# Optimization experiments

Hardware: AMD Instinct MI355X
Metric: run time of the kernel (lower is better)

## Reference

```python
import jax, jax.numpy as jnp
import numpy as np

B, T, I, H, C = 8192, 784, 1, 30, 10


def setup_inputs() -> dict:
    key = jax.random.key(0)
    ks = jax.random.split(key, 7)
    s_ih = 1.0 / np.sqrt(H)
    return {
        "x": jax.random.normal(ks[0], (B, T, I), dtype=jnp.float32),
        "W_ih": jax.random.uniform(ks[1], (H, I), jnp.float32, -s_ih, s_ih),
        "W_hh": jax.random.uniform(ks[2], (H, H), jnp.float32, -s_ih, s_ih),
        "b_ih": jax.random.uniform(ks[3], (H,), jnp.float32, -s_ih, s_ih),
        "b_hh": jax.random.uniform(ks[4], (H,), jnp.float32, -s_ih, s_ih),
        "W_fc": jax.random.uniform(ks[5], (C, H), jnp.float32, -s_ih, s_ih),
        "b_fc": jax.random.uniform(ks[6], (C,), jnp.float32, -s_ih, s_ih),
    }


def reference(x, W_ih, W_hh, b_ih, b_hh, W_fc, b_fc):
    # x: [B, T, I] -> scan over time. h_t = tanh(x_t W_ih^T + b_ih + h W_hh^T + b_hh)
    xs = jnp.swapaxes(x, 0, 1)  # [T, B, I]
    h0 = jnp.zeros((x.shape[0], W_hh.shape[0]), dtype=x.dtype)
    bias = b_ih + b_hh  # [H]

    def step(h, xt):
        h_new = jnp.tanh(xt @ W_ih.T + h @ W_hh.T + bias)
        return h_new, None

    hT, _ = jax.lax.scan(step, h0, xs)  # hT: [B, H] == out[:, -1, :]
    return hT @ W_fc.T + b_fc  # [B, C]
```

## Files before the change

kernel.cpp:

```cpp
#include <hip/hip_runtime.h>


#define BB 8192
#define TT 784
#define HH 30
#define CC 10

typedef __attribute__((ext_vector_type(8))) short  bf16x8;
typedef __attribute__((ext_vector_type(4))) float  f32x4;
typedef __attribute__((ext_vector_type(4))) unsigned uint4v;

__device__ __forceinline__ float tanh_pre(float s) {
    return 1.0f - 2.0f * __builtin_amdgcn_rcpf(__expf(s) + 1.0f);
}

#define BPAIR(p0, p1, hp, lp) do {                                          \
    asm("v_cvt_pk_bf16_f32 %0, %1, %2" : "=v"(hp) : "v"(p0), "v"(p1));      \
    const float _h0 = __uint_as_float((hp) << 16);                          \
    const float _h1 = __uint_as_float((hp) & 0xffff0000u);                  \
    const float _l0 = (p0) - _h0;                                           \
    const float _l1 = (p1) - _h1;                                           \
    asm("v_cvt_pk_bf16_f32 %0, %1, %2" : "=v"(lp) : "v"(_l0), "v"(_l1));    \
} while (0)

__global__ __launch_bounds__(64)
__attribute__((amdgpu_waves_per_eu(1, 1)))
void rnn_scan_kernel(const float* __restrict__ x,
                     const float* __restrict__ W_ih,
                     const float* __restrict__ W_hh,
                     const float* __restrict__ b_ih,
                     const float* __restrict__ b_hh,
                     const float* __restrict__ W_fc,
                     const float* __restrict__ b_fc,
                     float* __restrict__ out) {
    const int lane = threadIdx.x & 63;
    const int n    = lane & 15;
    const int g    = lane >> 4;
    const int b    = blockIdx.x * 16 + n;

    const int r1 = 8 * (n >> 2) + (n & 3);
    const int r2 = r1 + 4;
    unsigned a1h[4], a1l[4], a2h[4], a2l[4];
#pragma unroll
    for (int d = 0; d < 4; ++d) {
        const int k0 = 8 * g + 2 * d, k1 = k0 + 1;
        const float w1a = (k0 < HH) ? 2.0f * W_hh[r1 * HH + k0] : 0.f;
        const float w1b = (k1 < HH) ? 2.0f * W_hh[r1 * HH + k1] : 0.f;
        const float w2a = (r2 < HH && k0 < HH) ? 2.0f * W_hh[r2 * HH + k0] : 0.f;
        const float w2b = (r2 < HH && k1 < HH) ? 2.0f * W_hh[r2 * HH + k1] : 0.f;
        const unsigned u1a = __float_as_uint(w1a), u1b = __float_as_uint(w1b);
        const unsigned u2a = __float_as_uint(w2a), u2b = __float_as_uint(w2b);
        a1h[d] = (u1b & 0xffff0000u) | (u1a >> 16);
        a2h[d] = (u2b & 0xffff0000u) | (u2a >> 16);
        const float l1a = w1a - __uint_as_float(u1a & 0xffff0000u);
        const float l1b = w1b - __uint_as_float(u1b & 0xffff0000u);
        const float l2a = w2a - __uint_as_float(u2a & 0xffff0000u);
        const float l2b = w2b - __uint_as_float(u2b & 0xffff0000u);
        a1l[d] = (__float_as_uint(l1b) & 0xffff0000u) | (__float_as_uint(l1a) >> 16);
        a2l[d] = (__float_as_uint(l2b) & 0xffff0000u) | (__float_as_uint(l2a) >> 16);
    }
    bf16x8 A1h = __builtin_bit_cast(bf16x8, (uint4v){a1h[0], a1h[1], a1h[2], a1h[3]});
    bf16x8 A1l = __builtin_bit_cast(bf16x8, (uint4v){a1l[0], a1l[1], a1l[2], a1l[3]});
    bf16x8 A2h = __builtin_bit_cast(bf16x8, (uint4v){a2h[0], a2h[1], a2h[2], a2h[3]});
    bf16x8 A2l = __builtin_bit_cast(bf16x8, (uint4v){a2l[0], a2l[1], a2l[2], a2l[3]});
    asm volatile("" : "+v"(A1h), "+v"(A1l), "+v"(A2h), "+v"(A2l));

    float bias1[4], wih1[4], bias2[4], wih2[4];
#pragma unroll
    for (int r = 0; r < 4; ++r) {
        const int q1 = 8 * g + r;
        bias1[r] = 2.0f * (b_ih[q1] + b_hh[q1]);
        wih1[r]  = 2.0f * W_ih[q1];
        const int q2 = q1 + 4;
        bias2[r] = (q2 < HH) ? 2.0f * (b_ih[q2] + b_hh[q2]) : 0.f;
        wih2[r]  = (q2 < HH) ? 2.0f * W_ih[q2] : 0.f;
        asm volatile("" : "+v"(bias1[r]), "+v"(wih1[r]), "+v"(bias2[r]), "+v"(wih2[r]));
    }

    float h0 = 0.f, h1 = 0.f, h2 = 0.f, h3 = 0.f;
    float h4 = 0.f, h5 = 0.f, h6 = 0.f, h7 = 0.f;

    const float* xp = x + (size_t)b * TT;
    const int NQ = TT / 4;
    float4 xq = *(const float4*)xp;
    float4 xn = *(const float4*)(xp + 4);

    for (int qq = 0; qq < NQ; ++qq) {
        const float4 xf = (qq + 2 < NQ) ? *(const float4*)(xp + (qq + 2) * 4)
                                        : make_float4(0.f, 0.f, 0.f, 0.f);
#pragma unroll
        for (int u = 0; u < 4; ++u) {
            const float xt = (u == 0) ? xq.x : (u == 1) ? xq.y
                           : (u == 2) ? xq.z : xq.w;
            f32x4 accP1 = { fmaf(xt, wih1[0], bias1[0]), fmaf(xt, wih1[1], bias1[1]),
                            fmaf(xt, wih1[2], bias1[2]), fmaf(xt, wih1[3], bias1[3]) };
            f32x4 accP2 = { fmaf(xt, wih2[0], bias2[0]), fmaf(xt, wih2[1], bias2[1]),
                            fmaf(xt, wih2[2], bias2[2]), fmaf(xt, wih2[3], bias2[3]) };
            unsigned bh0, bh1, bh2, bh3, bl0, bl1, bl2, bl3;
            BPAIR(h0, h1, bh0, bl0);
            BPAIR(h2, h3, bh1, bl1);
            BPAIR(h4, h5, bh2, bl2);
            BPAIR(h6, h7, bh3, bl3);
            const bf16x8 Bh = __builtin_bit_cast(bf16x8, (uint4v){bh0, bh1, bh2, bh3});
            const bf16x8 Bl = __builtin_bit_cast(bf16x8, (uint4v){bl0, bl1, bl2, bl3});
            const f32x4 zed = {0.f, 0.f, 0.f, 0.f};
            accP1 = __builtin_amdgcn_mfma_f32_16x16x32_bf16(A1h, Bh, accP1, 0, 0, 0);
            accP2 = __builtin_amdgcn_mfma_f32_16x16x32_bf16(A2h, Bh, accP2, 0, 0, 0);
            f32x4 q1 = __builtin_amdgcn_mfma_f32_16x16x32_bf16(A1h, Bl, zed, 0, 0, 0);
            f32x4 q2 = __builtin_amdgcn_mfma_f32_16x16x32_bf16(A2h, Bl, zed, 0, 0, 0);
            q1 = __builtin_amdgcn_mfma_f32_16x16x32_bf16(A1l, Bh, q1, 0, 0, 0);
            q2 = __builtin_amdgcn_mfma_f32_16x16x32_bf16(A2l, Bh, q2, 0, 0, 0);
            const f32x4 s1 = accP1 + q1;
            const f32x4 s2 = accP2 + q2;
            h0 = tanh_pre(s1[0]); h1 = tanh_pre(s1[1]);
            h2 = tanh_pre(s1[2]); h3 = tanh_pre(s1[3]);
            h4 = tanh_pre(s2[0]); h5 = tanh_pre(s2[1]);
            h6 = tanh_pre(s2[2]); h7 = tanh_pre(s2[3]);
        }
        xq = xn;
        xn = xf;
    }

    const float hreg[8] = {h0, h1, h2, h3, h4, h5, h6, h7};
#pragma unroll
    for (int c = 0; c < CC; ++c) {
        float p = 0.f;
#pragma unroll
        for (int j = 0; j < 8; ++j) {
            const int k = 8 * g + j;
            if (k < HH) p = fmaf(W_fc[c * HH + k], hreg[j], p);
        }
        p += __shfl_xor(p, 16);
        p += __shfl_xor(p, 32);
        if (g == 0) out[(size_t)b * CC + c] = p + b_fc[c];
    }
}

extern "C" void kernel_launch(void* const* d_in, const int* in_sizes, int n_in,
                              void* d_out, int out_size, void* d_ws, size_t ws_size,
                              hipStream_t stream) {
    const float* x    = (const float*)d_in[0];
    const float* W_ih = (const float*)d_in[1];
    const float* W_hh = (const float*)d_in[2];
    const float* b_ih = (const float*)d_in[3];
    const float* b_hh = (const float*)d_in[4];
    const float* W_fc = (const float*)d_in[5];
    const float* b_fc = (const float*)d_in[6];

    hipLaunchKernelGGL(rnn_scan_kernel,
                       dim3(BB / 16), dim3(64), 0, stream,
                       x, W_ih, W_hh, b_ih, b_hh, W_fc, b_fc,
                       (float*)d_out);
}
```

Measured before the change: 287.2 us.

## Split hidden rows across two waves with LDS exchange of bf16 state

Each block now runs two waves, and each wave computes half of the hidden rows (one MFMA set instead of two). The packed bf16 hi/lo hidden state is exchanged through double-buffered shared memory with a block barrier every timestep. The weights are prescaled by 2/ln2 so tanh can use the exp2 builtin directly instead of __expf. The goal is to halve the per-wave serial MFMA and tanh latency per step, at the cost of an LDS round-trip and __syncthreads on the critical recurrence path.

```diff
diff --git a/kernel.cpp b/kernel.cpp
--- a/kernel.cpp
+++ b/kernel.cpp
@@ -10,8 +10,16 @@
 typedef __attribute__((ext_vector_type(4))) float  f32x4;
 typedef __attribute__((ext_vector_type(4))) unsigned uint4v;
 
-__device__ __forceinline__ float tanh_pre(float s) {
-    return 1.0f - 2.0f * __builtin_amdgcn_rcpf(__expf(s) + 1.0f);
+#if __has_builtin(__builtin_amdgcn_exp2f)
+#define EXP2(v) __builtin_amdgcn_exp2f(v)
+#else
+#define EXP2(v) __expf((v) * 0.69314718055994531f)
+#endif
+
+#define SCL 2.8853900817779268f
+
+__device__ __forceinline__ float tanh_e2(float s) {
+    return 1.0f - 2.0f * __builtin_amdgcn_rcpf(EXP2(s) + 1.0f);
 }
 
 #define BPAIR(p0, p1, hp, lp) do {                                          \
@@ -23,7 +31,7 @@
     asm("v_cvt_pk_bf16_f32 %0, %1, %2" : "=v"(lp) : "v"(_l0), "v"(_l1));    \
 } while (0)
 
-__global__ __launch_bounds__(64)
+__global__ __launch_bounds__(128)
 __attribute__((amdgpu_waves_per_eu(1, 1)))
 void rnn_scan_kernel(const float* __restrict__ x,
                      const float* __restrict__ W_ih,
@@ -33,52 +41,44 @@
                      const float* __restrict__ W_fc,
                      const float* __restrict__ b_fc,
                      float* __restrict__ out) {
-    const int lane = threadIdx.x & 63;
+    __shared__ unsigned long long Ehi[2][64][2];
+    __shared__ unsigned long long Elo[2][64][2];
+    __shared__ float hfc[16][33];
+
+    const int tid  = threadIdx.x;
+    const int wv   = tid >> 6;
+    const int lane = tid & 63;
     const int n    = lane & 15;
     const int g    = lane >> 4;
     const int b    = blockIdx.x * 16 + n;
 
-    const int r1 = 8 * (n >> 2) + (n & 3);
-    const int r2 = r1 + 4;
-    unsigned a1h[4], a1l[4], a2h[4], a2l[4];
+    const int rr = 8 * (n >> 2) + (n & 3) + 4 * wv;
+    unsigned ah[4], al[4];
 #pragma unroll
     for (int d = 0; d < 4; ++d) {
         const int k0 = 8 * g + 2 * d, k1 = k0 + 1;
-        const float w1a = (k0 < HH) ? 2.0f * W_hh[r1 * HH + k0] : 0.f;
-        const float w1b = (k1 < HH) ? 2.0f * W_hh[r1 * HH + k1] : 0.f;
-        const float w2a = (r2 < HH && k0 < HH) ? 2.0f * W_hh[r2 * HH + k0] : 0.f;
-        const float w2b = (r2 < HH && k1 < HH) ? 2.0f * W_hh[r2 * HH + k1] : 0.f;
-        const unsigned u1a = __float_as_uint(w1a), u1b = __float_as_uint(w1b);
-        const unsigned u2a = __float_as_uint(w2a), u2b = __float_as_uint(w2b);
-        a1h[d] = (u1b & 0xffff0000u) | (u1a >> 16);
-        a2h[d] = (u2b & 0xffff0000u) | (u2a >> 16);
-        const float l1a = w1a - __uint_as_float(u1a & 0xffff0000u);
-        const float l1b = w1b - __uint_as_float(u1b & 0xffff0000u);
-        const float l2a = w2a - __uint_as_float(u2a & 0xffff0000u);
-        const float l2b = w2b - __uint_as_float(u2b & 0xffff0000u);
-        a1l[d] = (__float_as_uint(l1b) & 0xffff0000u) | (__float_as_uint(l1a) >> 16);
-        a2l[d] = (__float_as_uint(l2b) & 0xffff0000u) | (__float_as_uint(l2a) >> 16);
+        const float wa = (rr < HH && k0 < HH) ? SCL * W_hh[rr * HH + k0] : 0.f;
+        const float wb = (rr < HH && k1 < HH) ? SCL * W_hh[rr * HH + k1] : 0.f;
+        const unsigned ua = __float_as_uint(wa), ub = __float_as_uint(wb);
+        ah[d] = (ub & 0xffff0000u) | (ua >> 16);
+        const float la = wa - __uint_as_float(ua & 0xffff0000u);
+        const float lb = wb - __uint_as_float(ub & 0xffff0000u);
+        al[d] = (__float_as_uint(lb) & 0xffff0000u) | (__float_as_uint(la) >> 16);
     }
-    bf16x8 A1h = __builtin_bit_cast(bf16x8, (uint4v){a1h[0], a1h[1], a1h[2], a1h[3]});
-    bf16x8 A1l = __builtin_bit_cast(bf16x8, (uint4v){a1l[0], a1l[1], a1l[2], a1l[3]});
-    bf16x8 A2h = __builtin_bit_cast(bf16x8, (uint4v){a2h[0], a2h[1], a2h[2], a2h[3]});
-    bf16x8 A2l = __builtin_bit_cast(bf16x8, (uint4v){a2l[0], a2l[1], a2l[2], a2l[3]});
-    asm volatile("" : "+v"(A1h), "+v"(A1l), "+v"(A2h), "+v"(A2l));
+    bf16x8 Ah = __builtin_bit_cast(bf16x8, (uint4v){ah[0], ah[1], ah[2], ah[3]});
+    bf16x8 Al = __builtin_bit_cast(bf16x8, (uint4v){al[0], al[1], al[2], al[3]});
+    asm volatile("" : "+v"(Ah), "+v"(Al));
 
-    float bias1[4], wih1[4], bias2[4], wih2[4];
+    float bias[4], wih[4];
 #pragma unroll
     for (int r = 0; r < 4; ++r) {
-        const int q1 = 8 * g + r;
-        bias1[r] = 2.0f * (b_ih[q1] + b_hh[q1]);
-        wih1[r]  = 2.0f * W_ih[q1];
-        const int q2 = q1 + 4;
-        bias2[r] = (q2 < HH) ? 2.0f * (b_ih[q2] + b_hh[q2]) : 0.f;
-        wih2[r]  = (q2 < HH) ? 2.0f * W_ih[q2] : 0.f;
-        asm volatile("" : "+v"(bias1[r]), "+v"(wih1[r]), "+v"(bias2[r]), "+v"(wih2[r]));
+        const int q = 8 * g + 4 * wv + r;
+        bias[r] = (q < HH) ? SCL * (b_ih[q] + b_hh[q]) : 0.f;
+        wih[r]  = (q < HH) ? SCL * W_ih[q] : 0.f;
+        asm volatile("" : "+v"(bias[r]), "+v"(wih[r]));
     }
 
     float h0 = 0.f, h1 = 0.f, h2 = 0.f, h3 = 0.f;
-    float h4 = 0.f, h5 = 0.f, h6 = 0.f, h7 = 0.f;
 
     const float* xp = x + (size_t)b * TT;
     const int NQ = TT / 4;
@@ -92,47 +92,50 @@
         for (int u = 0; u < 4; ++u) {
             const float xt = (u == 0) ? xq.x : (u == 1) ? xq.y
                            : (u == 2) ? xq.z : xq.w;
-            f32x4 accP1 = { fmaf(xt, wih1[0], bias1[0]), fmaf(xt, wih1[1], bias1[1]),
-                            fmaf(xt, wih1[2], bias1[2]), fmaf(xt, wih1[3], bias1[3]) };
-            f32x4 accP2 = { fmaf(xt, wih2[0], bias2[0]), fmaf(xt, wih2[1], bias2[1]),
-                            fmaf(xt, wih2[2], bias2[2]), fmaf(xt, wih2[3], bias2[3]) };
-            unsigned bh0, bh1, bh2, bh3, bl0, bl1, bl2, bl3;
-            BPAIR(h0, h1, bh0, bl0);
-            BPAIR(h2, h3, bh1, bl1);
-            BPAIR(h4, h5, bh2, bl2);
-            BPAIR(h6, h7, bh3, bl3);
-            const bf16x8 Bh = __builtin_bit_cast(bf16x8, (uint4v){bh0, bh1, bh2, bh3});
-            const bf16x8 Bl = __builtin_bit_cast(bf16x8, (uint4v){bl0, bl1, bl2, bl3});
+            const int buf = u & 1;
+            unsigned hp0, hp1, lp0, lp1;
+            BPAIR(h0, h1, hp0, lp0);
+            BPAIR(h2, h3, hp1, lp1);
+            Ehi[buf][lane][wv] = (unsigned long long)hp0 |
+                                 ((unsigned long long)hp1 << 32);
+            Elo[buf][lane][wv] = (unsigned long long)lp0 |
+                                 ((unsigned long long)lp1 << 32);
+            f32x4 acc = { fmaf(xt, wih[0], bias[0]), fmaf(xt, wih[1], bias[1]),
+                          fmaf(xt, wih[2], bias[2]), fmaf(xt, wih[3], bias[3]) };
+            __syncthreads();
+            const uint4v bhu = *(const uint4v*)&Ehi[buf][lane][0];
+            const uint4v blu = *(const uint4v*)&Elo[buf][lane][0];
+            const bf16x8 Bh = __builtin_bit_cast(bf16x8, bhu);
+            const bf16x8 Bl = __builtin_bit_cast(bf16x8, blu);
             const f32x4 zed = {0.f, 0.f, 0.f, 0.f};
-            accP1 = __builtin_amdgcn_mfma_f32_16x16x32_bf16(A1h, Bh, accP1, 0, 0, 0);
-            accP2 = __builtin_amdgcn_mfma_f32_16x16x32_bf16(A2h, Bh, accP2, 0, 0, 0);
-            f32x4 q1 = __builtin_amdgcn_mfma_f32_16x16x32_bf16(A1h, Bl, zed, 0, 0, 0);
-            f32x4 q2 = __builtin_amdgcn_mfma_f32_16x16x32_bf16(A2h, Bl, zed, 0, 0, 0);
-            q1 = __builtin_amdgcn_mfma_f32_16x16x32_bf16(A1l, Bh, q1, 0, 0, 0);
-            q2 = __builtin_amdgcn_mfma_f32_16x16x32_bf16(A2l, Bh, q2, 0, 0, 0);
-            const f32x4 s1 = accP1 + q1;
-            const f32x4 s2 = accP2 + q2;
-            h0 = tanh_pre(s1[0]); h1 = tanh_pre(s1[1]);
-            h2 = tanh_pre(s1[2]); h3 = tanh_pre(s1[3]);
-            h4 = tanh_pre(s2[0]); h5 = tanh_pre(s2[1]);
-            h6 = tanh_pre(s2[2]); h7 = tanh_pre(s2[3]);
+            acc = __builtin_amdgcn_mfma_f32_16x16x32_bf16(Ah, Bh, acc, 0, 0, 0);
+            f32x4 qv = __builtin_amdgcn_mfma_f32_16x16x32_bf16(Ah, Bl, zed, 0, 0, 0);
+            qv = __builtin_amdgcn_mfma_f32_16x16x32_bf16(Al, Bh, qv, 0, 0, 0);
+            const f32x4 s = acc + qv;
+            h0 = tanh_e2(s[0]); h1 = tanh_e2(s[1]);
+            h2 = tanh_e2(s[2]); h3 = tanh_e2(s[3]);
         }
         xq = xn;
         xn = xf;
     }
 
-    const float hreg[8] = {h0, h1, h2, h3, h4, h5, h6, h7};
+    hfc[n][8 * g + 4 * wv + 0] = h0;
+    hfc[n][8 * g + 4 * wv + 1] = h1;
+    hfc[n][8 * g + 4 * wv + 2] = h2;
+    hfc[n][8 * g + 4 * wv + 3] = h3;
+    __syncthreads();
+    if (wv == 0) {
 #pragma unroll
-    for (int c = 0; c < CC; ++c) {
-        float p = 0.f;
+        for (int j = 0; j < 3; ++j) {
+            const int c = g + 4 * j;
+            if (c < CC) {
+                float acc = b_fc[c];
 #pragma unroll
-        for (int j = 0; j < 8; ++j) {
-            const int k = 8 * g + j;
-            if (k < HH) p = fmaf(W_fc[c * HH + k], hreg[j], p);
+                for (int k = 0; k < HH; ++k)
+                    acc = fmaf(W_fc[c * HH + k], hfc[n][k], acc);
+                out[(size_t)b * CC + c] = acc;
+            }
         }
-        p += __shfl_xor(p, 16);
-        p += __shfl_xor(p, 32);
-        if (g == 0) out[(size_t)b * CC + c] = p + b_fc[c];
     }
 }
 
@@ -148,7 +151,7 @@
     const float* b_fc = (const float*)d_in[6];
 
     hipLaunchKernelGGL(rnn_scan_kernel,
-                       dim3(BB / 16), dim3(64), 0, stream,
+                       dim3(BB / 16), dim3(128), 0, stream,
                        x, W_ih, W_hh, b_ih, b_hh, W_fc, b_fc,
                        (float*)d_out);
 }
```

Result: faster. 273.6 us (-4.7%).
